# Optimization experiments

Measured on AMD Instinct MI355X. Metric: run time of the kernel, lower is better.

Reference implementation:

```python
import jax, jax.numpy as jnp
import numpy as np

N, D, F, C = 50000, 32, 128, 16
LN_EPS = 1e-5
CLAMP_MIN = 1e-5


def _layernorm_1d(x):
    # LayerNorm over the full node vector, no affine (elementwise_affine=False)
    m = x.mean()
    v = x.var()  # biased, matches torch LayerNorm
    return (x - m) / jnp.sqrt(v + LN_EPS)


def setup_inputs() -> dict:
    key = jax.random.key(0)
    k1, k2, k3, k4, k5, k6 = jax.random.split(key, 6)
    return {
        "h": jax.random.normal(k1, (N, F), dtype=jnp.float32),
        "logits": jax.random.normal(k2, (N, C), dtype=jnp.float32),
        "old_z": jax.random.uniform(k3, (N,), dtype=jnp.float32),
        "tau_1": jax.random.uniform(k4, (1,), dtype=jnp.float32),
        "tau_2": jax.random.uniform(k5, (1,), dtype=jnp.float32),
        "nbr": jax.random.randint(k6, (N, D), 0, N, dtype=jnp.int32),
    }


def reference(h, logits, old_z, tau_1, tau_2, nbr):
    # --- mailbox pass 1: neighbor logits -> adaptive gating features ---
    pred = jnp.argmax(logits[nbr], axis=2)          # [N, D] neighbor class preds
    center_pred = jnp.argmax(logits, axis=1)        # [N]
    # n_degree = 1 in the source (counts, not fractions) -- reproduced faithfully
    f1 = jnp.sum(pred == center_pred[:, None], axis=1).astype(h.dtype)  # [N]
    cnts = jax.nn.one_hot(pred, C, dtype=h.dtype).sum(axis=1)           # [N, C]
    cnts_p = jnp.clip(cnts, CLAMP_MIN, None)
    f2 = -jnp.sum(cnts_p * jnp.log(cnts_p), axis=1)                     # [N]
    f1 = jax.lax.stop_gradient(f1)
    f2 = jax.lax.stop_gradient(f2)

    norm_f1 = _layernorm_1d(f1)
    norm_f2 = _layernorm_1d(f2)
    # shared_tau=True path: tau_1, tau_2 passed in ([1] broadcasts over [N])
    z = jax.nn.sigmoid(-(norm_f1 - tau_1)) * jax.nn.sigmoid(-(norm_f2 - tau_2))  # [N]
    gate = jnp.minimum(old_z, z)

    # --- mailbox pass 2: scatter-sum of neighbor features ---
    agg = h[nbr].sum(axis=1)                        # [N, F]
    normagg = jax.nn.relu(agg)
    new_h = h + gate[:, None] * normagg
    return new_h, z
```

## Files before the change

### kernel.cpp

```cpp
#include <hip/hip_runtime.h>
#include <math.h>

#define NN 50000
#define DEG 32
#define FDIM 128
#define NCLS 16
#define LN_EPS 1e-5f
#define CLAMP_MIN 1e-5f

#define PRED_NB 196
#define CONV_NB 512
#define NGROUPS (NN * FDIM / 8)
#define FEAT_NB 196

#define SLICES 4
#define SL_U32 (NN * 16)
#define AGG_BPS ((NN * 4 + 255) / 256)
#define AGG_NB (SLICES * AGG_BPS)

typedef float  nf4 __attribute__((ext_vector_type(4)));
typedef unsigned nu4 __attribute__((ext_vector_type(4)));
typedef int    ni4 __attribute__((ext_vector_type(4)));

__device__ inline unsigned bf_rne(float x) {
    unsigned u = __float_as_uint(x);
    u += 0x7fffu + ((u >> 16) & 1u);
    return u >> 16;
}

__global__ __launch_bounds__(256) void k_pre(const float* __restrict__ logits,
                                             unsigned char* __restrict__ pred8,
                                             const float* __restrict__ h,
                                             unsigned* __restrict__ hb,
                                             float* __restrict__ acc4) {
    int b = blockIdx.x;
    if (b < PRED_NB) {
        if (b == 0 && threadIdx.x < 4) acc4[threadIdx.x] = 0.f;
        int i = b * 256 + threadIdx.x;
        if (i >= NN) return;
        const nf4* lp = (const nf4*)(logits + (long)i * NCLS);
        float best = -INFINITY;
        int bi = 0;
#pragma unroll
        for (int q = 0; q < 4; ++q) {
            nf4 v = __builtin_nontemporal_load(lp + q);
#pragma unroll
            for (int r = 0; r < 4; ++r) {
                if (v[r] > best) { best = v[r]; bi = q * 4 + r; }
            }
        }
        pred8[i] = (unsigned char)bi;
    } else {
        int g0 = (b - PRED_NB) * 256 + threadIdx.x;
        for (int g = g0; g < NGROUPS; g += CONV_NB * 256) {
            const nf4* src = (const nf4*)(h + (long)g * 8);
            nf4 a = __builtin_nontemporal_load(src);
            nf4 c = __builtin_nontemporal_load(src + 1);
            nu4 o;
            o.x = bf_rne(a.x) | (bf_rne(a.y) << 16);
            o.y = bf_rne(a.z) | (bf_rne(a.w) << 16);
            o.z = bf_rne(c.x) | (bf_rne(c.y) << 16);
            o.w = bf_rne(c.z) | (bf_rne(c.w) << 16);
            int node = g >> 4;
            int q    = (g >> 2) & 3;
            int sub  = g & 3;
            ((nu4*)hb)[(size_t)q * (NN * 4) + node * 4 + sub] = o;
        }
    }
}

__global__ __launch_bounds__(256) void k_feats_lds(const int* __restrict__ nbr,
                                                   const unsigned char* __restrict__ pred8,
                                                   float* __restrict__ f1,
                                                   float* __restrict__ f2,
                                                   float* __restrict__ acc4, int n) {
    __shared__ unsigned char lp[NN];
    {
        const uint4* s4 = (const uint4*)pred8;
        uint4* d4 = (uint4*)lp;
        for (int i = threadIdx.x; i < 3125; i += 256) d4[i] = s4[i];
    }
    __syncthreads();
    int node = blockIdx.x * 256 + threadIdx.x;
    float v1 = 0.f, v2 = 0.f;
    if (node < n) {
        unsigned long long lo = 0ull, hi = 0ull;
        const ni4* np = (const ni4*)(nbr + (long)node * DEG);
#pragma unroll
        for (int q = 0; q < 8; ++q) {
            ni4 k4 = __builtin_nontemporal_load(np + q);
            int ks[4] = {k4.x, k4.y, k4.z, k4.w};
#pragma unroll
            for (int r = 0; r < 4; ++r) {
                int p = lp[ks[r]];
                unsigned long long inc = 1ull << ((p & 7) * 8);
                if (p < 8) lo += inc; else hi += inc;
            }
        }
        int cp = lp[node];
        unsigned long long src = (cp < 8) ? lo : hi;
        v1 = (float)((src >> ((cp & 7) * 8)) & 0xffull);
        float ent = 0.f;
#pragma unroll
        for (int c = 0; c < NCLS; ++c) {
            unsigned long long s = (c < 8) ? lo : hi;
            float cnt = (float)((s >> ((c & 7) * 8)) & 0xffull);
            float x = fmaxf(cnt, CLAMP_MIN);
            ent -= x * __logf(x);
        }
        v2 = ent;
        f1[node] = v1;
        f2[node] = v2;
    }
    float s0 = v1, s1 = v1 * v1, s2 = v2, s3 = v2 * v2;
#pragma unroll
    for (int off = 32; off > 0; off >>= 1) {
        s0 += __shfl_down(s0, off);
        s1 += __shfl_down(s1, off);
        s2 += __shfl_down(s2, off);
        s3 += __shfl_down(s3, off);
    }
    __shared__ float red[4][4];
    int wid = threadIdx.x >> 6;
    if ((threadIdx.x & 63) == 0) {
        red[wid][0] = s0; red[wid][1] = s1; red[wid][2] = s2; red[wid][3] = s3;
    }
    __syncthreads();
    if (threadIdx.x == 0) {
        float t0 = 0.f, t1 = 0.f, t2 = 0.f, t3 = 0.f;
#pragma unroll
        for (int w = 0; w < 4; ++w) {
            t0 += red[w][0]; t1 += red[w][1]; t2 += red[w][2]; t3 += red[w][3];
        }
        atomicAdd(&acc4[0], t0);
        atomicAdd(&acc4[1], t1);
        atomicAdd(&acc4[2], t2);
        atomicAdd(&acc4[3], t3);
    }
}

#define U2F(x) __uint_as_float(x)

#define ISSUE(buf, base) do {                                                   \
    buf[0] = ((const nu4*)(slab + (size_t)kk[(base) + 0] * 16))[lane];          \
    buf[1] = ((const nu4*)(slab + (size_t)kk[(base) + 1] * 16))[lane];          \
    buf[2] = ((const nu4*)(slab + (size_t)kk[(base) + 2] * 16))[lane];          \
    buf[3] = ((const nu4*)(slab + (size_t)kk[(base) + 3] * 16))[lane];          \
} while (0)

#define CONSUME(buf) do {                                                       \
    _Pragma("unroll")                                                           \
    for (int s2 = 0; s2 < 4; ++s2) {                                            \
        acc[0] += U2F(buf[s2].x << 16); acc[1] += U2F(buf[s2].x & 0xffff0000u); \
        acc[2] += U2F(buf[s2].y << 16); acc[3] += U2F(buf[s2].y & 0xffff0000u); \
        acc[4] += U2F(buf[s2].z << 16); acc[5] += U2F(buf[s2].z & 0xffff0000u); \
        acc[6] += U2F(buf[s2].w << 16); acc[7] += U2F(buf[s2].w & 0xffff0000u); \
    }                                                                           \
} while (0)

__global__ __launch_bounds__(256) void k_agg_sl(const unsigned* __restrict__ hb,
                                                const int* __restrict__ nbr,
                                                const float* __restrict__ old_z,
                                                const float* __restrict__ tau1,
                                                const float* __restrict__ tau2,
                                                const float* __restrict__ f1,
                                                const float* __restrict__ f2,
                                                const float* __restrict__ acc4,
                                                float* __restrict__ out_h,
                                                float* __restrict__ out_z, int n) {
    int q = blockIdx.x / AGG_BPS;
    int t = (blockIdx.x - q * AGG_BPS) * 256 + threadIdx.x;
    int node = t >> 2;
    int lane = t & 3;
    if (node >= n) return;
    const unsigned* slab = hb + (size_t)q * SL_U32;

    double inv_n = 1.0 / (double)NN;
    double m1 = (double)acc4[0] * inv_n;
    double var1 = (double)acc4[1] * inv_n - m1 * m1;
    double m2 = (double)acc4[2] * inv_n;
    double var2 = (double)acc4[3] * inv_n - m2 * m2;
    float p0 = (float)m1, p1 = (float)(1.0 / sqrt(var1 + (double)LN_EPS));
    float p2 = (float)m2, p3 = (float)(1.0 / sqrt(var2 + (double)LN_EPS));

    const ni4* np = (const ni4*)(nbr + (long)node * DEG);
    int kk[32];
#pragma unroll
    for (int j = 0; j < 8; ++j) {
        ni4 v = np[j];
        kk[4 * j + 0] = v.x; kk[4 * j + 1] = v.y;
        kk[4 * j + 2] = v.z; kk[4 * j + 3] = v.w;
    }

    float acc[8];
#pragma unroll
    for (int i = 0; i < 8; ++i) acc[i] = 0.f;

    nu4 A[4], B[4];
    ISSUE(A, 0);  ISSUE(B, 4);
    CONSUME(A);   ISSUE(A, 8);
    CONSUME(B);   ISSUE(B, 12);
    CONSUME(A);   ISSUE(A, 16);
    CONSUME(B);   ISSUE(B, 20);
    CONSUME(A);   ISSUE(A, 24);
    CONSUME(B);   ISSUE(B, 28);
    CONSUME(A);   CONSUME(B);

    float a = (f1[node] - p0) * p1 - tau1[0];
    float b = (f2[node] - p2) * p3 - tau2[0];
    float z = 1.f / ((1.f + expf(a)) * (1.f + expf(b)));
    float gate = fminf(old_z[node], z);

    nu4 hid = ((const nu4*)(slab + (size_t)node * 16))[lane];
    nf4 o0, o1;
    o0.x = U2F(hid.x << 16)          + gate * fmaxf(acc[0], 0.f);
    o0.y = U2F(hid.x & 0xffff0000u)  + gate * fmaxf(acc[1], 0.f);
    o0.z = U2F(hid.y << 16)          + gate * fmaxf(acc[2], 0.f);
    o0.w = U2F(hid.y & 0xffff0000u)  + gate * fmaxf(acc[3], 0.f);
    o1.x = U2F(hid.z << 16)          + gate * fmaxf(acc[4], 0.f);
    o1.y = U2F(hid.z & 0xffff0000u)  + gate * fmaxf(acc[5], 0.f);
    o1.z = U2F(hid.w << 16)          + gate * fmaxf(acc[6], 0.f);
    o1.w = U2F(hid.w & 0xffff0000u)  + gate * fmaxf(acc[7], 0.f);
    nf4* op = (nf4*)(out_h + (long)node * FDIM + q * 32 + lane * 8);
    __builtin_nontemporal_store(o0, op);
    __builtin_nontemporal_store(o1, op + 1);
    if (q == 0 && lane == 0) __builtin_nontemporal_store(z, out_z + node);
}

extern "C" void kernel_launch(void* const* d_in, const int* in_sizes, int n_in,
                              void* d_out, int out_size, void* d_ws, size_t ws_size,
                              hipStream_t stream) {
    const float* h      = (const float*)d_in[0];
    const float* logits = (const float*)d_in[1];
    const float* old_z  = (const float*)d_in[2];
    const float* tau1   = (const float*)d_in[3];
    const float* tau2   = (const float*)d_in[4];
    const int*   nbr    = (const int*)d_in[5];

    char* ws = (char*)d_ws;
    float*         acc4   = (float*)ws;
    unsigned char* pred8  = (unsigned char*)(ws + 32768);
    float*         f1     = (float*)(ws + 90112);
    float*         f2     = (float*)(ws + 294912);
    unsigned*      hb     = (unsigned*)(ws + 524288);

    float* out_h = (float*)d_out;
    float* out_z = out_h + (long)NN * FDIM;

    k_pre      <<<PRED_NB + CONV_NB, 256, 0, stream>>>(logits, pred8, h, hb, acc4);
    k_feats_lds<<<FEAT_NB, 256, 0, stream>>>(nbr, pred8, f1, f2, acc4, NN);
    k_agg_sl   <<<AGG_NB, 256, 0, stream>>>(hb, nbr, old_z, tau1, tau2,
                                            f1, f2, acc4, out_h, out_z, NN);
}
```

Baseline: 155.2 us.

## Quantize neighbor features to int8 with per-node scales, halve slice count

Replaces the bf16 copy of h with an int8 copy that has a per-node 8-bit scale code, halving the bytes fetched per neighbor gather. The aggregation now uses two 64-feature slices instead of four 32-feature slices, and each agg block stages the whole 50KB scale table into LDS. The residual term now reads the exact fp32 h. This trades gather bandwidth for lower accumulation precision, extra dequantize ALU work, and an LDS fill in every block that may limit occupancy.

```diff
diff --git a/kernel.cpp b/kernel.cpp
--- a/kernel.cpp
+++ b/kernel.cpp
@@ -9,29 +9,24 @@
 #define CLAMP_MIN 1e-5f
 
 #define PRED_NB 196
-#define CONV_NB 512
-#define NGROUPS (NN * FDIM / 8)
+#define CONV_NB 782
 #define FEAT_NB 196
 
-#define SLICES 4
+#define SLICES 2
 #define SL_U32 (NN * 16)
 #define AGG_BPS ((NN * 4 + 255) / 256)
 #define AGG_NB (SLICES * AGG_BPS)
+#define SDEC(e) ((float)((e) + 1) * (8.0f / 32512.0f))
 
 typedef float  nf4 __attribute__((ext_vector_type(4)));
 typedef unsigned nu4 __attribute__((ext_vector_type(4)));
 typedef int    ni4 __attribute__((ext_vector_type(4)));
-
-__device__ inline unsigned bf_rne(float x) {
-    unsigned u = __float_as_uint(x);
-    u += 0x7fffu + ((u >> 16) & 1u);
-    return u >> 16;
-}
 
 __global__ __launch_bounds__(256) void k_pre(const float* __restrict__ logits,
                                              unsigned char* __restrict__ pred8,
                                              const float* __restrict__ h,
                                              unsigned* __restrict__ hb,
+                                             unsigned char* __restrict__ sc8,
                                              float* __restrict__ acc4) {
     int b = blockIdx.x;
     if (b < PRED_NB) {
@@ -51,21 +46,43 @@
         }
         pred8[i] = (unsigned char)bi;
     } else {
-        int g0 = (b - PRED_NB) * 256 + threadIdx.x;
-        for (int g = g0; g < NGROUPS; g += CONV_NB * 256) {
-            const nf4* src = (const nf4*)(h + (long)g * 8);
-            nf4 a = __builtin_nontemporal_load(src);
-            nf4 c = __builtin_nontemporal_load(src + 1);
-            nu4 o;
-            o.x = bf_rne(a.x) | (bf_rne(a.y) << 16);
-            o.y = bf_rne(a.z) | (bf_rne(a.w) << 16);
-            o.z = bf_rne(c.x) | (bf_rne(c.y) << 16);
-            o.w = bf_rne(c.z) | (bf_rne(c.w) << 16);
-            int node = g >> 4;
-            int q    = (g >> 2) & 3;
-            int sub  = g & 3;
-            ((nu4*)hb)[(size_t)q * (NN * 4) + node * 4 + sub] = o;
-        }
+        int g = (b - PRED_NB) * 256 + threadIdx.x;
+        if (g >= NN * 4) return;
+        int node = g >> 2, l = g & 3;
+        const nf4* hp = (const nf4*)(h + (size_t)node * FDIM + l * 32);
+        nf4 v[8];
+        float m = 0.f;
+#pragma unroll
+        for (int j = 0; j < 8; ++j) {
+            v[j] = __builtin_nontemporal_load(hp + j);
+#pragma unroll
+            for (int r = 0; r < 4; ++r) m = fmaxf(m, __builtin_fabsf(v[j][r]));
+        }
+        m = fmaxf(m, __shfl_xor(m, 1));
+        m = fmaxf(m, __shfl_xor(m, 2));
+        int e = (int)ceilf(m * 32.0f) - 1;
+        e = max(0, min(255, e));
+        float s = SDEC(e);
+        float inv_s = 1.0f / s;
+        unsigned w[8];
+#pragma unroll
+        for (int j = 0; j < 8; ++j) {
+            unsigned ww = 0;
+#pragma unroll
+            for (int r = 0; r < 4; ++r) {
+                float qf = fminf(fmaxf(v[j][r] * inv_s, -127.f), 127.f);
+                int qi = __float2int_rn(qf);
+                ww |= ((unsigned)qi & 0xffu) << (8 * r);
+            }
+            w[j] = ww;
+        }
+        unsigned* dst = hb + ((size_t)(l >> 1) * NN + (size_t)node) * 16 + (l & 1) * 8;
+        nu4 o0, o1;
+        o0.x = w[0]; o0.y = w[1]; o0.z = w[2]; o0.w = w[3];
+        o1.x = w[4]; o1.y = w[5]; o1.z = w[6]; o1.w = w[7];
+        ((nu4*)dst)[0] = o0;
+        ((nu4*)dst)[1] = o1;
+        if (l == 0) sc8[node] = (unsigned char)e;
     }
 }
 
@@ -139,8 +156,6 @@
     }
 }
 
-#define U2F(x) __uint_as_float(x)
-
 #define ISSUE(buf, base) do {                                                   \
     buf[0] = ((const nu4*)(slab + (size_t)kk[(base) + 0] * 16))[lane];          \
     buf[1] = ((const nu4*)(slab + (size_t)kk[(base) + 1] * 16))[lane];          \
@@ -148,18 +163,26 @@
     buf[3] = ((const nu4*)(slab + (size_t)kk[(base) + 3] * 16))[lane];          \
 } while (0)
 
-#define CONSUME(buf) do {                                                       \
+#define DEC_ADD(w, o, s) do {                                                   \
+    acc[(o)+0] = fmaf((float)(int)(signed char)((w)      ), (s), acc[(o)+0]);   \
+    acc[(o)+1] = fmaf((float)(int)(signed char)((w) >>  8), (s), acc[(o)+1]);   \
+    acc[(o)+2] = fmaf((float)(int)(signed char)((w) >> 16), (s), acc[(o)+2]);   \
+    acc[(o)+3] = fmaf((float)(int)(signed char)((w) >> 24), (s), acc[(o)+3]);   \
+} while (0)
+
+#define CONSUME(buf, base) do {                                                 \
     _Pragma("unroll")                                                           \
     for (int s2 = 0; s2 < 4; ++s2) {                                            \
-        acc[0] += U2F(buf[s2].x << 16); acc[1] += U2F(buf[s2].x & 0xffff0000u); \
-        acc[2] += U2F(buf[s2].y << 16); acc[3] += U2F(buf[s2].y & 0xffff0000u); \
-        acc[4] += U2F(buf[s2].z << 16); acc[5] += U2F(buf[s2].z & 0xffff0000u); \
-        acc[6] += U2F(buf[s2].w << 16); acc[7] += U2F(buf[s2].w & 0xffff0000u); \
+        float sc = SDEC((int)lsc[kk[(base) + s2]]);                             \
+        DEC_ADD(buf[s2].x, 0, sc);  DEC_ADD(buf[s2].y, 4, sc);                  \
+        DEC_ADD(buf[s2].z, 8, sc);  DEC_ADD(buf[s2].w, 12, sc);                 \
     }                                                                           \
 } while (0)
 
 __global__ __launch_bounds__(256) void k_agg_sl(const unsigned* __restrict__ hb,
+                                                const unsigned char* __restrict__ sc8,
                                                 const int* __restrict__ nbr,
+                                                const float* __restrict__ h,
                                                 const float* __restrict__ old_z,
                                                 const float* __restrict__ tau1,
                                                 const float* __restrict__ tau2,
@@ -168,6 +191,14 @@
                                                 const float* __restrict__ acc4,
                                                 float* __restrict__ out_h,
                                                 float* __restrict__ out_z, int n) {
+    __shared__ unsigned char lsc[NN];
+    {
+        const uint4* s4 = (const uint4*)sc8;
+        uint4* d4 = (uint4*)lsc;
+        for (int i = threadIdx.x; i < 3125; i += 256) d4[i] = s4[i];
+    }
+    __syncthreads();
+
     int q = blockIdx.x / AGG_BPS;
     int t = (blockIdx.x - q * AGG_BPS) * 256 + threadIdx.x;
     int node = t >> 2;
@@ -192,38 +223,37 @@
         kk[4 * j + 2] = v.z; kk[4 * j + 3] = v.w;
     }
 
-    float acc[8];
-#pragma unroll
-    for (int i = 0; i < 8; ++i) acc[i] = 0.f;
+    float acc[16];
+#pragma unroll
+    for (int i = 0; i < 16; ++i) acc[i] = 0.f;
 
     nu4 A[4], B[4];
-    ISSUE(A, 0);  ISSUE(B, 4);
-    CONSUME(A);   ISSUE(A, 8);
-    CONSUME(B);   ISSUE(B, 12);
-    CONSUME(A);   ISSUE(A, 16);
-    CONSUME(B);   ISSUE(B, 20);
-    CONSUME(A);   ISSUE(A, 24);
-    CONSUME(B);   ISSUE(B, 28);
-    CONSUME(A);   CONSUME(B);
+    ISSUE(A, 0);      ISSUE(B, 4);
+    CONSUME(A, 0);    ISSUE(A, 8);
+    CONSUME(B, 4);    ISSUE(B, 12);
+    CONSUME(A, 8);    ISSUE(A, 16);
+    CONSUME(B, 12);   ISSUE(B, 20);
+    CONSUME(A, 16);   ISSUE(A, 24);
+    CONSUME(B, 20);   ISSUE(B, 28);
+    CONSUME(A, 24);   CONSUME(B, 28);
 
     float a = (f1[node] - p0) * p1 - tau1[0];
     float b = (f2[node] - p2) * p3 - tau2[0];
     float z = 1.f / ((1.f + expf(a)) * (1.f + expf(b)));
     float gate = fminf(old_z[node], z);
 
-    nu4 hid = ((const nu4*)(slab + (size_t)node * 16))[lane];
-    nf4 o0, o1;
-    o0.x = U2F(hid.x << 16)          + gate * fmaxf(acc[0], 0.f);
-    o0.y = U2F(hid.x & 0xffff0000u)  + gate * fmaxf(acc[1], 0.f);
-    o0.z = U2F(hid.y << 16)          + gate * fmaxf(acc[2], 0.f);
-    o0.w = U2F(hid.y & 0xffff0000u)  + gate * fmaxf(acc[3], 0.f);
-    o1.x = U2F(hid.z << 16)          + gate * fmaxf(acc[4], 0.f);
-    o1.y = U2F(hid.z & 0xffff0000u)  + gate * fmaxf(acc[5], 0.f);
-    o1.z = U2F(hid.w << 16)          + gate * fmaxf(acc[6], 0.f);
-    o1.w = U2F(hid.w & 0xffff0000u)  + gate * fmaxf(acc[7], 0.f);
-    nf4* op = (nf4*)(out_h + (long)node * FDIM + q * 32 + lane * 8);
-    __builtin_nontemporal_store(o0, op);
-    __builtin_nontemporal_store(o1, op + 1);
+    const nf4* hid4 = (const nf4*)(h + (long)node * FDIM + q * 64 + lane * 16);
+    nf4* op = (nf4*)(out_h + (long)node * FDIM + q * 64 + lane * 16);
+#pragma unroll
+    for (int v4 = 0; v4 < 4; ++v4) {
+        nf4 hid = hid4[v4];
+        nf4 o;
+        o.x = hid.x + gate * fmaxf(acc[v4 * 4 + 0], 0.f);
+        o.y = hid.y + gate * fmaxf(acc[v4 * 4 + 1], 0.f);
+        o.z = hid.z + gate * fmaxf(acc[v4 * 4 + 2], 0.f);
+        o.w = hid.w + gate * fmaxf(acc[v4 * 4 + 3], 0.f);
+        __builtin_nontemporal_store(o, op + v4);
+    }
     if (q == 0 && lane == 0) __builtin_nontemporal_store(z, out_z + node);
 }
 
@@ -242,13 +272,14 @@
     unsigned char* pred8  = (unsigned char*)(ws + 32768);
     float*         f1     = (float*)(ws + 90112);
     float*         f2     = (float*)(ws + 294912);
-    unsigned*      hb     = (unsigned*)(ws + 524288);
+    unsigned char* sc8    = (unsigned char*)(ws + 524288);
+    unsigned*      hb     = (unsigned*)(ws + 589824);
 
     float* out_h = (float*)d_out;
     float* out_z = out_h + (long)NN * FDIM;
 
-    k_pre      <<<PRED_NB + CONV_NB, 256, 0, stream>>>(logits, pred8, h, hb, acc4);
+    k_pre      <<<PRED_NB + CONV_NB, 256, 0, stream>>>(logits, pred8, h, hb, sc8, acc4);
     k_feats_lds<<<FEAT_NB, 256, 0, stream>>>(nbr, pred8, f1, f2, acc4, NN);
-    k_agg_sl   <<<AGG_NB, 256, 0, stream>>>(hb, nbr, old_z, tau1, tau2,
+    k_agg_sl   <<<AGG_NB, 256, 0, stream>>>(hb, sc8, nbr, h, old_z, tau1, tau2,
                                             f1, f2, acc4, out_h, out_z, NN);
 }
```

New measurement: 158.2 us. No clear change (+1.9%).
